# Performance work log

Hardware: AMD Instinct MI355X
Metric: run time of the kernel (lower is better)

The kernel has to match this reference:

```python
import jax, jax.numpy as jnp
import numpy as np

B, T, H = 16, 64, 1024          # batch, src/target length, decoder hidden
D = 2 * H                        # encoder hidden dim (bidirectional)
EMB = 512                        # embedding size
MAX_OUT = 1024                   # maxout units
VOCAB = 32000


def setup_inputs() -> dict:
    key = jax.random.key(0)
    ks = jax.random.split(key, 16)
    s = 0.02
    return {
        "h": jax.random.normal(ks[0], (B, T, D), dtype=jnp.float32),
        # Alignment: nn_h (2H -> T), nn_s (H -> T)  (FCNN with no hidden layers = Linear)
        "W_h": jax.random.normal(ks[1], (D, T), dtype=jnp.float32) * s,
        "b_h": jnp.zeros((T,), dtype=jnp.float32),
        "W_s": jax.random.normal(ks[2], (H, T), dtype=jnp.float32) * s,
        "b_s": jnp.zeros((T,), dtype=jnp.float32),
        # GRU cell (PyTorch layout, stored transposed: [in, 3H] / [H, 3H], gate order r,z,n)
        "W_ih": jax.random.normal(ks[3], (D, 3 * H), dtype=jnp.float32) * s,
        "b_ih": jnp.zeros((3 * H,), dtype=jnp.float32),
        "W_hh": jax.random.normal(ks[4], (H, 3 * H), dtype=jnp.float32) * s,
        "b_hh": jnp.zeros((3 * H,), dtype=jnp.float32),
        # embedding FCNN: H -> EMB
        "W_emb": jax.random.normal(ks[5], (H, EMB), dtype=jnp.float32) * s,
        "b_emb": jnp.zeros((EMB,), dtype=jnp.float32),
        # OutputNetwork t_nn: (EMB + 3H) -> 2*MAX_OUT ; output_nn: MAX_OUT -> VOCAB
        "W_t": jax.random.normal(ks[6], (EMB + 3 * H, 2 * MAX_OUT), dtype=jnp.float32) * s,
        "b_t": jnp.zeros((2 * MAX_OUT,), dtype=jnp.float32),
        "W_out": jax.random.normal(ks[7], (MAX_OUT, VOCAB), dtype=jnp.float32) * s,
        "b_out": jnp.zeros((VOCAB,), dtype=jnp.float32),
    }


def reference(h, W_h, b_h, W_s, b_s, W_ih, b_ih, W_hh, b_hh,
              W_emb, b_emb, W_t, b_t, W_out, b_out):
    Bq, Tq, Dq = h.shape
    Hq = W_hh.shape[0]
    # precompute encoder projection for alignment: [B, T, T]
    h_emb = h @ W_h + b_h

    def step(s, he_i):
        # s: [B, H] decoder state; he_i: [B, T]
        a = jnp.tanh(s @ W_s + b_s + he_i)          # Alignment (tanh)
        e = jax.nn.softmax(a, axis=1)               # [B, T] attention weights
        c = jnp.einsum("btd,bt->bd", h, e)          # context [B, 2H]
        # GRU cell (torch semantics, gates r,z,n)
        gi = c @ W_ih + b_ih
        gh = s @ W_hh + b_hh
        ir, iz, inn = jnp.split(gi, 3, axis=1)
        hr, hz, hn = jnp.split(gh, 3, axis=1)
        r = jax.nn.sigmoid(ir + hr)
        z = jax.nn.sigmoid(iz + hz)
        n = jnp.tanh(inn + r * hn)
        s_new = (1.0 - z) * n + z * s               # new state == GRU output (1 layer)
        y_emb = s_new @ W_emb + b_emb               # embedding FCNN of raw_y_i
        t_tilde = jnp.concatenate([s_new, y_emb, c], axis=1) @ W_t + b_t
        M = t_tilde.shape[1] // 2
        t = jnp.maximum(t_tilde[:, :M], t_tilde[:, M:])  # maxout over halves
        out = t @ W_out + b_out                     # [B, VOCAB]
        return s_new, out

    s0 = jnp.zeros((Bq, Hq), dtype=h.dtype)
    _, outs = jax.lax.scan(step, s0, jnp.swapaxes(h_emb, 0, 1))  # outs: [T, B, V]
    return jnp.swapaxes(outs, 0, 1)                               # [B, T, V]
```

## Files before the change

kernel.cpp:

```cpp
#include <hip/hip_runtime.h>
#include <stdint.h>


typedef __attribute__((ext_vector_type(8))) short bf16x8;
typedef __attribute__((ext_vector_type(4))) float f32x4;

__device__ __forceinline__ uint16_t f2b(float x) {
  uint32_t u = __float_as_uint(x);
  return (uint16_t)((u + 0x7FFFu + ((u >> 16) & 1u)) >> 16);
}
__device__ __forceinline__ float b2f(uint16_t x) {
  return __uint_as_float(((uint32_t)x) << 16);
}

struct us4 { uint16_t a, b, c, d; };

__global__ void k_cvt_bf16(const float* __restrict__ in, uint16_t* __restrict__ out, int n4) {
  int i = blockIdx.x * 256 + threadIdx.x;
  if (i >= n4) return;
  float4 v = ((const float4*)in)[i];
  us4 o; o.a = f2b(v.x); o.b = f2b(v.y); o.c = f2b(v.z); o.d = f2b(v.w);
  ((us4*)out)[i] = o;
}

__global__ void k_transpose_bf16(const float* __restrict__ in, uint16_t* __restrict__ out,
                                 int R, int C) {
  __shared__ float tile[32][33];
  int c0 = blockIdx.x * 32, r0 = blockIdx.y * 32;
  int tx = threadIdx.x & 31, ty = threadIdx.x >> 5;
  #pragma unroll
  for (int i = 0; i < 4; ++i) {
    int r = ty + i * 8;
    tile[r][tx] = in[(size_t)(r0 + r) * C + c0 + tx];
  }
  __syncthreads();
  #pragma unroll
  for (int i = 0; i < 4; ++i) {
    int r = ty + i * 8;
    out[(size_t)(c0 + r) * R + r0 + tx] = f2b(tile[tx][r]);
  }
}

template<int MODE>
__global__ __launch_bounds__(256) void k_gemm(
    const uint16_t* __restrict__ A, int lda,
    const uint16_t* __restrict__ BT, int ldb,
    void* __restrict__ C, int ldc, const float* __restrict__ bias,
    int M, int N, int K) {
  __shared__ uint16_t sA[128 * 64];
  __shared__ uint16_t sB[128 * 64];
  const int tid = threadIdx.x;
  const int wave = tid >> 6, lane = tid & 63;
  const int r16 = lane & 15, g = lane >> 4;
  const int wr = wave >> 1, wc = wave & 1;
  const int m0 = blockIdx.y * 128, n0 = blockIdx.x * 128;
  f32x4 acc[4][4] = {};
  for (int k0 = 0; k0 < K; k0 += 64) {
    __syncthreads();
    #pragma unroll
    for (int i = 0; i < 4; ++i) {
      int chunk = wave * 256 + i * 64 + lane;
      int row = chunk >> 3, c8 = chunk & 7;
      int arow = m0 + row; arow = arow < M ? arow : M - 1;
      int brow = n0 + row; brow = brow < N ? brow : N - 1;
      const uint16_t* ga = A + (size_t)arow * lda + k0 + c8 * 8;
      const uint16_t* gb = BT + (size_t)brow * ldb + k0 + c8 * 8;
      uint16_t* la = sA + (size_t)(wave * 256 + i * 64) * 8;
      uint16_t* lb = sB + (size_t)(wave * 256 + i * 64) * 8;
      __builtin_amdgcn_global_load_lds((const __attribute__((address_space(1))) void*)ga,
                                       (__attribute__((address_space(3))) void*)la, 16, 0, 0);
      __builtin_amdgcn_global_load_lds((const __attribute__((address_space(1))) void*)gb,
                                       (__attribute__((address_space(3))) void*)lb, 16, 0, 0);
    }
    __syncthreads();
    #pragma unroll
    for (int kk = 0; kk < 2; ++kk) {
      bf16x8 af[4], bfr[4];
      #pragma unroll
      for (int mi = 0; mi < 4; ++mi)
        af[mi] = *(const bf16x8*)&sA[(wr * 64 + mi * 16 + r16) * 64 + kk * 32 + g * 8];
      #pragma unroll
      for (int ni = 0; ni < 4; ++ni)
        bfr[ni] = *(const bf16x8*)&sB[(wc * 64 + ni * 16 + r16) * 64 + kk * 32 + g * 8];
      #pragma unroll
      for (int mi = 0; mi < 4; ++mi)
        #pragma unroll
        for (int ni = 0; ni < 4; ++ni)
          acc[mi][ni] = __builtin_amdgcn_mfma_f32_16x16x32_bf16(af[mi], bfr[ni], acc[mi][ni], 0, 0, 0);
    }
  }
  #pragma unroll
  for (int mi = 0; mi < 4; ++mi) {
    #pragma unroll
    for (int ni = 0; ni < 4; ++ni) {
      int col = n0 + wc * 64 + ni * 16 + r16;
      if (col >= N) continue;
      float bv = bias ? bias[col] : 0.0f;
      #pragma unroll
      for (int r = 0; r < 4; ++r) {
        int row = m0 + wr * 64 + mi * 16 + 4 * g + r;
        if (row >= M) continue;
        float v = acc[mi][ni][r] + bv;
        if (MODE == 0) {
          ((float*)C)[(size_t)row * ldc + col] = v;
        } else if (MODE == 1) {
          ((uint16_t*)C)[(size_t)row * ldc + col] = f2b(v);
        } else {
          int tstep = row >> 4, bb = row & 15;
          ((float*)C)[(size_t)(bb * 64 + tstep) * ldc + col] = v;
        }
      }
    }
  }
}

__global__ void k_maxout(const float* __restrict__ tt, uint16_t* __restrict__ tout) {
  int i = blockIdx.x * 256 + threadIdx.x;
  int m = i >> 10, n = i & 1023;
  tout[i] = f2b(fmaxf(tt[(size_t)m * 2048 + n], tt[(size_t)m * 2048 + 1024 + n]));
}

struct ScanParams {
  const uint16_t* h_bf;
  const uint16_t* WsT;
  const uint16_t* WhhT;
  const uint16_t* Hih;
  const float* hemb;
  const float* b_s; const float* b_ih; const float* b_hh;
  float* abuf;
  float* gi;
  float* gh;
  float* sf0; float* sf1;
  uint16_t* sb;
  uint16_t* X;
};

__global__ __launch_bounds__(256) void k_stepA(ScanParams p, int t) {
  const int bid = blockIdx.x, tid = threadIdx.x;
  __shared__ float s_new[1024];
  const int b = bid >> 2, tc = (bid & 3) << 4;
  if (t > 0) {
    const float* sfr = ((t - 1) & 1) ? p.sf1 : p.sf0;
    float* sfw = (t & 1) ? p.sf1 : p.sf0;
    #pragma unroll
    for (int u = 0; u < 4; ++u) {
      int j = tid + u * 256;
      float ir = p.gi[b * 3072 + j],         hr = p.gh[b * 3072 + j];
      float iz = p.gi[b * 3072 + 1024 + j],  hz = p.gh[b * 3072 + 1024 + j];
      float in_ = p.gi[b * 3072 + 2048 + j], hn = p.gh[b * 3072 + 2048 + j];
      float rr = 1.0f / (1.0f + __expf(-(ir + hr)));
      float zz = 1.0f / (1.0f + __expf(-(iz + hz)));
      float nn = tanhf(in_ + rr * hn);
      float sv = (1.0f - zz) * nn + zz * sfr[b * 1024 + j];
      s_new[j] = sv;
      if ((bid & 3) == 0) {
        sfw[b * 1024 + j] = sv;
        p.sb[b * 1024 + j] = f2b(sv);
        p.X[(size_t)((t - 1) * 16 + b) * 3584 + j] = f2b(sv);
      }
    }
  } else {
    #pragma unroll
    for (int u = 0; u < 4; ++u) {
      int j = tid + u * 256;
      s_new[j] = 0.0f;
      if ((bid & 3) == 0) { p.sf0[b * 1024 + j] = 0.0f; p.sb[b * 1024 + j] = 0; }
    }
  }
  __syncthreads();
  int tp = tid >> 4, kl = tid & 15;
  const uint16_t* wrow = p.WsT + (size_t)(tc + tp) * 1024;
  float av = 0.0f;
  for (int u = 0; u < 64; ++u) { int k = kl + u * 16; av += s_new[k] * b2f(wrow[k]); }
  av += __shfl_xor(av, 8, 16);
  av += __shfl_xor(av, 4, 16);
  av += __shfl_xor(av, 2, 16);
  av += __shfl_xor(av, 1, 16);
  if (kl == 0) {
    int tg = tc + tp;
    p.abuf[b * 64 + tg] = tanhf(av + p.b_s[tg] + p.hemb[(size_t)(b * 64 + t) * 64 + tg]);
  }
}

__global__ __launch_bounds__(256) void k_stepFinal(ScanParams p) {
  const int b = blockIdx.x, tid = threadIdx.x;
  #pragma unroll
  for (int u = 0; u < 4; ++u) {
    int j = tid + u * 256;
    float ir = p.gi[b * 3072 + j],         hr = p.gh[b * 3072 + j];
    float iz = p.gi[b * 3072 + 1024 + j],  hz = p.gh[b * 3072 + 1024 + j];
    float in_ = p.gi[b * 3072 + 2048 + j], hn = p.gh[b * 3072 + 2048 + j];
    float rr = 1.0f / (1.0f + __expf(-(ir + hr)));
    float zz = 1.0f / (1.0f + __expf(-(iz + hz)));
    float nn = tanhf(in_ + rr * hn);
    float sv = (1.0f - zz) * nn + zz * p.sf1[b * 1024 + j];
    p.X[(size_t)(63 * 16 + b) * 3584 + j] = f2b(sv);
  }
}

__device__ __forceinline__ void softmax64(const float* __restrict__ arow, float* e_lds, int tid) {
  if (tid < 64) {
    float v = arow[tid];
    float m = v;
    #pragma unroll
    for (int mask = 32; mask; mask >>= 1) m = fmaxf(m, __shfl_xor(m, mask));
    float pv = __expf(v - m);
    float s = pv;
    #pragma unroll
    for (int mask = 32; mask; mask >>= 1) s += __shfl_xor(s, mask);
    e_lds[tid] = pv / s;
  }
  __syncthreads();
}

__global__ __launch_bounds__(256) void k_stepB(ScanParams p, int t) {
  const int bid = blockIdx.x, tid = threadIdx.x;
  __shared__ float e_lds[64];
  __shared__ float red[512];
  if (bid < 96) {
    const int wave = tid >> 6, lane = tid & 63;
    const int r16 = lane & 15, g = lane >> 4;
    const int sub = wave & 1, kh = wave >> 1;
    const int n0 = (bid * 2 + sub) * 16;
    f32x4 acc = {};
    #pragma unroll 4
    for (int ks = 0; ks < 16; ++ks) {
      int k = kh * 512 + ks * 32 + g * 8;
      bf16x8 a = *(const bf16x8*)&p.sb[r16 * 1024 + k];
      bf16x8 bb = *(const bf16x8*)&p.WhhT[(size_t)(n0 + r16) * 1024 + k];
      acc = __builtin_amdgcn_mfma_f32_16x16x32_bf16(a, bb, acc, 0, 0, 0);
    }
    if (kh == 1) {
      #pragma unroll
      for (int r = 0; r < 4; ++r) red[sub * 256 + lane * 4 + r] = acc[r];
    }
    __syncthreads();
    if (kh == 0) {
      #pragma unroll
      for (int r = 0; r < 4; ++r) {
        float v = acc[r] + red[sub * 256 + lane * 4 + r];
        int row = 4 * g + r, col = n0 + r16;
        p.gh[row * 3072 + col] = v + p.b_hh[col];
      }
    }
  } else if (bid < 864) {
    const int idx = bid - 96, b = idx / 48, c0 = (idx % 48) * 64;
    softmax64(p.abuf + b * 64, e_lds, tid);
    const int col = c0 + (tid & 63), q = tid >> 6;
    float av = 0.0f;
    #pragma unroll
    for (int u = 0; u < 16; ++u) {
      int ts = q * 16 + u;
      av += e_lds[ts] * b2f(p.Hih[(size_t)(b * 64 + ts) * 3072 + col]);
    }
    red[q * 64 + (tid & 63)] = av;
    __syncthreads();
    if (tid < 64) {
      float v = red[tid] + red[64 + tid] + red[128 + tid] + red[192 + tid];
      p.gi[b * 3072 + c0 + tid] = v + p.b_ih[c0 + tid];
    }
  } else {
    const int idx = bid - 864, b = idx >> 3, d0 = (idx & 7) * 256;
    softmax64(p.abuf + b * 64, e_lds, tid);
    float av = 0.0f;
    #pragma unroll 8
    for (int ts = 0; ts < 64; ++ts)
      av += e_lds[ts] * b2f(p.h_bf[(size_t)(b * 64 + ts) * 2048 + d0 + tid]);
    p.X[(size_t)(t * 16 + b) * 3584 + 1536 + d0 + tid] = f2b(av);
  }
}

extern "C" void kernel_launch(void* const* d_in, const int* in_sizes, int n_in,
                              void* d_out, int out_size, void* d_ws, size_t ws_size,
                              hipStream_t stream) {
  const float* h     = (const float*)d_in[0];
  const float* W_h   = (const float*)d_in[1];
  const float* b_h   = (const float*)d_in[2];
  const float* W_s   = (const float*)d_in[3];
  const float* b_s   = (const float*)d_in[4];
  const float* W_ih  = (const float*)d_in[5];
  const float* b_ih  = (const float*)d_in[6];
  const float* W_hh  = (const float*)d_in[7];
  const float* b_hh  = (const float*)d_in[8];
  const float* W_emb = (const float*)d_in[9];
  const float* b_emb = (const float*)d_in[10];
  const float* W_t   = (const float*)d_in[11];
  const float* b_t   = (const float*)d_in[12];
  const float* W_out = (const float*)d_in[13];
  const float* b_out = (const float*)d_in[14];

  char* base = (char*)d_ws; size_t off = 0;
  auto alloc = [&](size_t bytes) -> void* {
    off = (off + 255) & ~(size_t)255;
    void* pp = base + off; off += bytes; return pp;
  };
  uint16_t* h_bf  = (uint16_t*)alloc((size_t)1024 * 2048 * 2);
  uint16_t* WhT   = (uint16_t*)alloc((size_t)64 * 2048 * 2);
  uint16_t* WsT   = (uint16_t*)alloc((size_t)64 * 1024 * 2);
  uint16_t* WhhT  = (uint16_t*)alloc((size_t)3072 * 1024 * 2);
  uint16_t* WihT  = (uint16_t*)alloc((size_t)3072 * 2048 * 2);
  uint16_t* WembT = (uint16_t*)alloc((size_t)512 * 1024 * 2);
  uint16_t* WtT   = (uint16_t*)alloc((size_t)2048 * 3584 * 2);
  uint16_t* WoutT = (uint16_t*)alloc((size_t)32000 * 1024 * 2);
  float*    hemb  = (float*)alloc((size_t)1024 * 64 * 4);
  uint16_t* Hih   = (uint16_t*)alloc((size_t)1024 * 3072 * 2);
  uint16_t* X     = (uint16_t*)alloc((size_t)1024 * 3584 * 2);
  float*    tt    = (float*)alloc((size_t)1024 * 2048 * 4);
  uint16_t* t_all = (uint16_t*)alloc((size_t)1024 * 1024 * 2);
  float*    abuf  = (float*)alloc((size_t)16 * 64 * 4);
  float*    gi    = (float*)alloc((size_t)16 * 3072 * 4);
  float*    gh    = (float*)alloc((size_t)16 * 3072 * 4);
  float*    sf0   = (float*)alloc((size_t)16 * 1024 * 4);
  float*    sf1   = (float*)alloc((size_t)16 * 1024 * 4);
  uint16_t* sb    = (uint16_t*)alloc((size_t)16 * 1024 * 2);

  k_cvt_bf16<<<2048, 256, 0, stream>>>(h, h_bf, 1024 * 2048 / 4);
  k_transpose_bf16<<<dim3(2, 64), 256, 0, stream>>>(W_h, WhT, 2048, 64);
  k_transpose_bf16<<<dim3(2, 32), 256, 0, stream>>>(W_s, WsT, 1024, 64);
  k_transpose_bf16<<<dim3(96, 32), 256, 0, stream>>>(W_hh, WhhT, 1024, 3072);
  k_transpose_bf16<<<dim3(96, 64), 256, 0, stream>>>(W_ih, WihT, 2048, 3072);
  k_transpose_bf16<<<dim3(16, 32), 256, 0, stream>>>(W_emb, WembT, 1024, 512);
  k_transpose_bf16<<<dim3(64, 112), 256, 0, stream>>>(W_t, WtT, 3584, 2048);
  k_transpose_bf16<<<dim3(1000, 32), 256, 0, stream>>>(W_out, WoutT, 1024, 32000);

  k_gemm<0><<<dim3(1, 8), 256, 0, stream>>>(h_bf, 2048, WhT, 2048, hemb, 64, b_h, 1024, 64, 2048);
  k_gemm<1><<<dim3(24, 8), 256, 0, stream>>>(h_bf, 2048, WihT, 2048, Hih, 3072, nullptr, 1024, 3072, 2048);

  ScanParams sp{h_bf, WsT, WhhT, Hih, hemb, b_s, b_ih, b_hh, abuf, gi, gh, sf0, sf1, sb, X};
  for (int t = 0; t < 64; ++t) {
    k_stepA<<<64, 256, 0, stream>>>(sp, t);
    k_stepB<<<992, 256, 0, stream>>>(sp, t);
  }
  k_stepFinal<<<16, 256, 0, stream>>>(sp);

  k_gemm<1><<<dim3(4, 8), 256, 0, stream>>>(X, 3584, WembT, 1024, X + 1024, 3584, b_emb, 1024, 512, 1024);
  k_gemm<0><<<dim3(16, 8), 256, 0, stream>>>(X, 3584, WtT, 3584, tt, 2048, b_t, 1024, 2048, 3584);
  k_maxout<<<4096, 256, 0, stream>>>(tt, t_all);
  k_gemm<2><<<dim3(250, 8), 256, 0, stream>>>(t_all, 1024, WoutT, 1024, (float*)d_out, 32000, b_out, 1024, 32000, 1024);
}
```

Before: 1.494 ms.

## Fuse per-timestep scan launches into one cooperative kernel with grid syncs

Replaces the 129 separate step kernel launches of the recurrent scan with a single cooperative kernel of 256 blocks. Each timestep runs the stepA and stepB work, separated by grid-wide barriers, and each block loops over up to four virtual stepB blocks. The old launches remain as a fallback if the cooperative launch fails. The GEMM grid mapping is also swapped so that consecutive blocks walk along M, which changes L2 reuse of the weight tiles. The aim is to remove per-launch overhead, at the cost of grid-sync latency and fewer resident blocks for the stepB work.

```diff
diff --git a/kernel.cpp b/kernel.cpp
--- a/kernel.cpp
+++ b/kernel.cpp
@@ -1,5 +1,8 @@
 #include <hip/hip_runtime.h>
+#include <hip/hip_cooperative_groups.h>
 #include <stdint.h>
+
+namespace cg = cooperative_groups;
 
 
 typedef __attribute__((ext_vector_type(8))) short bf16x8;
@@ -53,7 +56,7 @@
   const int wave = tid >> 6, lane = tid & 63;
   const int r16 = lane & 15, g = lane >> 4;
   const int wr = wave >> 1, wc = wave & 1;
-  const int m0 = blockIdx.y * 128, n0 = blockIdx.x * 128;
+  const int m0 = blockIdx.x * 128, n0 = blockIdx.y * 128;
   f32x4 acc[4][4] = {};
   for (int k0 = 0; k0 < K; k0 += 64) {
     __syncthreads();
@@ -135,10 +138,10 @@
   uint16_t* X;
 };
 
-__global__ __launch_bounds__(256) void k_stepA(ScanParams p, int t) {
-  const int bid = blockIdx.x, tid = threadIdx.x;
-  __shared__ float s_new[1024];
-  const int b = bid >> 2, tc = (bid & 3) << 4;
+
+__device__ __forceinline__ void stepA_body(const ScanParams& p, int t, int v, int tid,
+                                           float* s_new) {
+  const int b = v >> 2, tc = (v & 3) << 4;
   if (t > 0) {
     const float* sfr = ((t - 1) & 1) ? p.sf1 : p.sf0;
     float* sfw = (t & 1) ? p.sf1 : p.sf0;
@@ -153,7 +156,7 @@
       float nn = tanhf(in_ + rr * hn);
       float sv = (1.0f - zz) * nn + zz * sfr[b * 1024 + j];
       s_new[j] = sv;
-      if ((bid & 3) == 0) {
+      if ((v & 3) == 0) {
         sfw[b * 1024 + j] = sv;
         p.sb[b * 1024 + j] = f2b(sv);
         p.X[(size_t)((t - 1) * 16 + b) * 3584 + j] = f2b(sv);
@@ -164,7 +167,7 @@
     for (int u = 0; u < 4; ++u) {
       int j = tid + u * 256;
       s_new[j] = 0.0f;
-      if ((bid & 3) == 0) { p.sf0[b * 1024 + j] = 0.0f; p.sb[b * 1024 + j] = 0; }
+      if ((v & 3) == 0) { p.sf0[b * 1024 + j] = 0.0f; p.sb[b * 1024 + j] = 0; }
     }
   }
   __syncthreads();
@@ -182,8 +185,23 @@
   }
 }
 
-__global__ __launch_bounds__(256) void k_stepFinal(ScanParams p) {
-  const int b = blockIdx.x, tid = threadIdx.x;
+__device__ __forceinline__ void softmax64(const float* __restrict__ arow, float* e_lds, int tid) {
+  if (tid < 64) {
+    float v = arow[tid];
+    float m = v;
+    #pragma unroll
+    for (int mask = 32; mask; mask >>= 1) m = fmaxf(m, __shfl_xor(m, mask));
+    float pv = __expf(v - m);
+    float s = pv;
+    #pragma unroll
+    for (int mask = 32; mask; mask >>= 1) s += __shfl_xor(s, mask);
+    e_lds[tid] = pv / s;
+  }
+  __syncthreads();
+}
+
+__device__ __forceinline__ void stepFinal_body(const ScanParams& p, int v, int tid) {
+  const int b = v;
   #pragma unroll
   for (int u = 0; u < 4; ++u) {
     int j = tid + u * 256;
@@ -198,30 +216,13 @@
   }
 }
 
-__device__ __forceinline__ void softmax64(const float* __restrict__ arow, float* e_lds, int tid) {
-  if (tid < 64) {
-    float v = arow[tid];
-    float m = v;
-    #pragma unroll
-    for (int mask = 32; mask; mask >>= 1) m = fmaxf(m, __shfl_xor(m, mask));
-    float pv = __expf(v - m);
-    float s = pv;
-    #pragma unroll
-    for (int mask = 32; mask; mask >>= 1) s += __shfl_xor(s, mask);
-    e_lds[tid] = pv / s;
-  }
-  __syncthreads();
-}
-
-__global__ __launch_bounds__(256) void k_stepB(ScanParams p, int t) {
-  const int bid = blockIdx.x, tid = threadIdx.x;
-  __shared__ float e_lds[64];
-  __shared__ float red[512];
-  if (bid < 96) {
+__device__ __forceinline__ void stepB_body(const ScanParams& p, int t, int v, int tid,
+                                           float* e_lds, float* red) {
+  if (v < 96) {
     const int wave = tid >> 6, lane = tid & 63;
     const int r16 = lane & 15, g = lane >> 4;
     const int sub = wave & 1, kh = wave >> 1;
-    const int n0 = (bid * 2 + sub) * 16;
+    const int n0 = (v * 2 + sub) * 16;
     f32x4 acc = {};
     #pragma unroll 4
     for (int ks = 0; ks < 16; ++ks) {
@@ -238,13 +239,13 @@
     if (kh == 0) {
       #pragma unroll
       for (int r = 0; r < 4; ++r) {
-        float v = acc[r] + red[sub * 256 + lane * 4 + r];
+        float vv = acc[r] + red[sub * 256 + lane * 4 + r];
         int row = 4 * g + r, col = n0 + r16;
-        p.gh[row * 3072 + col] = v + p.b_hh[col];
+        p.gh[row * 3072 + col] = vv + p.b_hh[col];
       }
     }
-  } else if (bid < 864) {
-    const int idx = bid - 96, b = idx / 48, c0 = (idx % 48) * 64;
+  } else if (v < 864) {
+    const int idx = v - 96, b = idx / 48, c0 = (idx % 48) * 64;
     softmax64(p.abuf + b * 64, e_lds, tid);
     const int col = c0 + (tid & 63), q = tid >> 6;
     float av = 0.0f;
@@ -256,11 +257,11 @@
     red[q * 64 + (tid & 63)] = av;
     __syncthreads();
     if (tid < 64) {
-      float v = red[tid] + red[64 + tid] + red[128 + tid] + red[192 + tid];
-      p.gi[b * 3072 + c0 + tid] = v + p.b_ih[c0 + tid];
+      float vv = red[tid] + red[64 + tid] + red[128 + tid] + red[192 + tid];
+      p.gi[b * 3072 + c0 + tid] = vv + p.b_ih[c0 + tid];
     }
   } else {
-    const int idx = bid - 864, b = idx >> 3, d0 = (idx & 7) * 256;
+    const int idx = v - 864, b = idx >> 3, d0 = (idx & 7) * 256;
     softmax64(p.abuf + b * 64, e_lds, tid);
     float av = 0.0f;
     #pragma unroll 8
@@ -268,6 +269,42 @@
       av += e_lds[ts] * b2f(p.h_bf[(size_t)(b * 64 + ts) * 2048 + d0 + tid]);
     p.X[(size_t)(t * 16 + b) * 3584 + 1536 + d0 + tid] = f2b(av);
   }
+}
+
+__global__ __launch_bounds__(256) void k_scan_fused(ScanParams p) {
+  cg::grid_group grid = cg::this_grid();
+  const int bid = blockIdx.x, tid = threadIdx.x;
+  __shared__ float s_new[1024];
+  __shared__ float e_lds[64];
+  __shared__ float red[512];
+
+  for (int t = 0; t < 64; ++t) {
+    if (bid < 64) stepA_body(p, t, bid, tid, s_new);
+    grid.sync();
+    #pragma unroll
+    for (int i = 0; i < 4; ++i) {
+      int v = bid + i * 256;
+      if (v < 992) stepB_body(p, t, v, tid, e_lds, red);
+      __syncthreads();
+    }
+    grid.sync();
+  }
+  if (bid < 16) stepFinal_body(p, bid, tid);
+}
+
+__global__ __launch_bounds__(256) void k_stepA(ScanParams p, int t) {
+  __shared__ float s_new[1024];
+  stepA_body(p, t, blockIdx.x, threadIdx.x, s_new);
+}
+
+__global__ __launch_bounds__(256) void k_stepB(ScanParams p, int t) {
+  __shared__ float e_lds[64];
+  __shared__ float red[512];
+  stepB_body(p, t, blockIdx.x, threadIdx.x, e_lds, red);
+}
+
+__global__ __launch_bounds__(256) void k_stepFinal(ScanParams p) {
+  stepFinal_body(p, blockIdx.x, threadIdx.x);
 }
 
 extern "C" void kernel_launch(void* const* d_in, const int* in_sizes, int n_in,
@@ -323,18 +360,23 @@
   k_transpose_bf16<<<dim3(64, 112), 256, 0, stream>>>(W_t, WtT, 3584, 2048);
   k_transpose_bf16<<<dim3(1000, 32), 256, 0, stream>>>(W_out, WoutT, 1024, 32000);
 
-  k_gemm<0><<<dim3(1, 8), 256, 0, stream>>>(h_bf, 2048, WhT, 2048, hemb, 64, b_h, 1024, 64, 2048);
-  k_gemm<1><<<dim3(24, 8), 256, 0, stream>>>(h_bf, 2048, WihT, 2048, Hih, 3072, nullptr, 1024, 3072, 2048);
+  k_gemm<0><<<dim3(8, 1), 256, 0, stream>>>(h_bf, 2048, WhT, 2048, hemb, 64, b_h, 1024, 64, 2048);
+  k_gemm<1><<<dim3(8, 24), 256, 0, stream>>>(h_bf, 2048, WihT, 2048, Hih, 3072, nullptr, 1024, 3072, 2048);
 
   ScanParams sp{h_bf, WsT, WhhT, Hih, hemb, b_s, b_ih, b_hh, abuf, gi, gh, sf0, sf1, sb, X};
-  for (int t = 0; t < 64; ++t) {
-    k_stepA<<<64, 256, 0, stream>>>(sp, t);
-    k_stepB<<<992, 256, 0, stream>>>(sp, t);
-  }
-  k_stepFinal<<<16, 256, 0, stream>>>(sp);
-
-  k_gemm<1><<<dim3(4, 8), 256, 0, stream>>>(X, 3584, WembT, 1024, X + 1024, 3584, b_emb, 1024, 512, 1024);
-  k_gemm<0><<<dim3(16, 8), 256, 0, stream>>>(X, 3584, WtT, 3584, tt, 2048, b_t, 1024, 2048, 3584);
+  void* args[] = {&sp};
+  hipError_t cerr = hipLaunchCooperativeKernel((void*)k_scan_fused, dim3(256), dim3(256),
+                                               args, 0, stream);
+  if (cerr != hipSuccess) {
+    for (int t = 0; t < 64; ++t) {
+      k_stepA<<<64, 256, 0, stream>>>(sp, t);
+      k_stepB<<<992, 256, 0, stream>>>(sp, t);
+    }
+    k_stepFinal<<<16, 256, 0, stream>>>(sp);
+  }
+
+  k_gemm<1><<<dim3(8, 4), 256, 0, stream>>>(X, 3584, WembT, 1024, X + 1024, 3584, b_emb, 1024, 512, 1024);
+  k_gemm<0><<<dim3(8, 16), 256, 0, stream>>>(X, 3584, WtT, 3584, tt, 2048, b_t, 1024, 2048, 3584);
   k_maxout<<<4096, 256, 0, stream>>>(tt, t_all);
-  k_gemm<2><<<dim3(250, 8), 256, 0, stream>>>(t_all, 1024, WoutT, 1024, (float*)d_out, 32000, b_out, 1024, 32000, 1024);
-}
+  k_gemm<2><<<dim3(8, 250), 256, 0, stream>>>(t_all, 1024, WoutT, 1024, (float*)d_out, 32000, b_out, 1024, 32000, 1024);
+}
```

New measurement: 5.376 ms. 260% more time.
